# Kernel optimization log

Measured on AMD Instinct MI355X. Metric: run time of the kernel, lower is better.

Reference implementation:

```python
import jax, jax.numpy as jnp
import numpy as np

B, T, D, NH = 4, 2048, 1024, 16
HD = D // NH


def setup_inputs() -> dict:
    key = jax.random.key(0)
    ks = jax.random.split(key, 6)
    scale = 0.02
    x = jax.random.normal(ks[0], (B, T, D), dtype=jnp.float32)
    Wr = jax.random.normal(ks[1], (D, D), dtype=jnp.float32) * scale
    Wk = jax.random.normal(ks[2], (D, D), dtype=jnp.float32) * scale
    Wv = jax.random.normal(ks[3], (D, D), dtype=jnp.float32) * scale
    Ww = jax.random.normal(ks[4], (D, D), dtype=jnp.float32) * scale
    Wo = jax.random.normal(ks[5], (D, D), dtype=jnp.float32) * scale
    return {"x": x, "Wr": Wr, "Wk": Wk, "Wv": Wv, "Ww": Ww, "Wo": Wo}


def _rwkv7_forward(x, Wr, Wk, Wv, Ww, Wo):
    b, t, d = x.shape
    nh, hd = NH, d // NH
    # projections (F.linear: x @ W.T), no bias
    r = jax.nn.sigmoid(x @ Wr.T).reshape(b, t, nh, hd)
    k = (x @ Wk.T).reshape(b, t, nh, hd)
    v = (x @ Wv.T).reshape(b, t, nh, hd)
    w = (jax.nn.sigmoid(x @ Ww.T) * 0.99).reshape(b, t, nh, hd)

    def step(state, inp):
        # state: [B, nh, hd_v, hd_k]
        w_t, k_t, v_t, r_t = inp  # each [B, nh, hd]
        state = state * w_t[..., :, None] + v_t[..., :, None] * k_t[..., None, :]
        out_t = r_t * state.sum(-1)  # [B, nh, hd]
        return state, out_t

    seq = (jnp.moveaxis(w, 1, 0), jnp.moveaxis(k, 1, 0),
           jnp.moveaxis(v, 1, 0), jnp.moveaxis(r, 1, 0))  # time-major
    state0 = jnp.zeros((b, nh, hd, hd), dtype=x.dtype)
    _, outs = jax.lax.scan(step, state0, seq)  # [T, B, nh, hd]
    out = jnp.moveaxis(outs, 0, 1).reshape(b, t, d)

    # RMSNorm with eps=None -> torch uses dtype eps
    eps = jnp.asarray(jnp.finfo(out.dtype).eps, out.dtype)
    out = out * jax.lax.rsqrt(jnp.mean(out * out, axis=-1, keepdims=True) + eps)
    return out @ Wo.T


def reference(x, Wr, Wk, Wv, Ww, Wo):
    return _rwkv7_forward(x, Wr, Wk, Wv, Ww, Wo)
```

## Files before the change

### kernel.cpp

```cpp
#include <hip/hip_runtime.h>
#include <hip/hip_bf16.h>
#include <stdint.h>


#define BB 4
#define TT 2048
#define DD 1024
#define NHH 16
#define HDD 64
#define CC 64
#define LL 32
#define NCH 4096
#define MT (BB * TT)
#define ROWP 136

using bf16 = __hip_bfloat16;
typedef __attribute__((ext_vector_type(8))) short bfrag8;
typedef __attribute__((ext_vector_type(8))) unsigned short us8;
typedef __attribute__((ext_vector_type(4))) float f32x4;

__device__ __forceinline__ void async_ld16(const bf16* g, bf16* l) {
  __builtin_amdgcn_global_load_lds(
      (const __attribute__((address_space(1))) uint32_t*)g,
      (__attribute__((address_space(3))) uint32_t*)l, 16, 0, 0);
}

__device__ __forceinline__ float sigm(float x) {
  return __builtin_amdgcn_rcpf(1.0f + __expf(-x));
}
__device__ __forceinline__ float bf2f(bf16 h) {
  unsigned short u = *reinterpret_cast<unsigned short*>(&h);
  return __uint_as_float((unsigned)u << 16);
}
__device__ __forceinline__ float us2f(unsigned short u) {
  return __uint_as_float((unsigned)u << 16);
}
__device__ __forceinline__ unsigned short f2bfbits(float f) {
  bf16 b = __float2bfloat16(f);
  return *reinterpret_cast<unsigned short*>(&b);
}

__global__ __launch_bounds__(256)
void convert_kernel(const float* __restrict__ x,
                    const float* __restrict__ Wr, const float* __restrict__ Wv,
                    const float* __restrict__ Ww, const float* __restrict__ Wo,
                    const float* __restrict__ Wk,
                    bf16* __restrict__ x_c, bf16* __restrict__ W_c,
                    bf16* __restrict__ wks_bf)
{
  if (blockIdx.x < 64) {
    const int gid = blockIdx.x * 256 + threadIdx.x;
    const int h = gid >> 10, c = gid & 1023;
    float s = 0.0f;
    for (int j = 0; j < 64; ++j)
      s += Wk[(long)((h << 6) + j) * 1024 + c];
    wks_bf[gid] = __float2bfloat16(s);
    return;
  }
  const long g = (long)(blockIdx.x - 64) * 256 + threadIdx.x;
  const float* src; bf16* dst; long off4;
  if (g < 2097152) { src = x; dst = x_c; off4 = g; }
  else {
    long gg = g - 2097152;
    int wsel = (int)(gg >> 18);
    off4 = gg & 262143;
    src = (wsel == 0) ? Wr : (wsel == 1) ? Wv : (wsel == 2) ? Ww : Wo;
    dst = W_c + (long)wsel * 1048576;
  }
  float4 f = reinterpret_cast<const float4*>(src)[off4];
  ushort4 pk;
  pk.x = f2bfbits(f.x); pk.y = f2bfbits(f.y);
  pk.z = f2bfbits(f.z); pk.w = f2bfbits(f.w);
  reinterpret_cast<ushort4*>(dst)[off4] = pk;
}

__device__ __forceinline__ void gemm_mainloop(
    const bf16* __restrict__ A, const bf16* __restrict__ W,
    int blockM, int blockN, bf16* a_sh, bf16* b_sh, f32x4 acc[4][4])
{
  const int tid    = threadIdx.x;
  const int wave   = tid >> 6;
  const int lane   = tid & 63;
  const int lane15 = lane & 15;
  const int quad   = lane >> 4;
  const int waveM  = wave >> 1;
  const int waveN  = wave & 1;
  const int s_row  = (wave << 5) + (lane >> 3);
  const int s_col  = (((lane & 7) ^ ((lane >> 3) & 7)) << 3);

  const bf16* gA = A + ((long)(blockM * 128) + s_row) * 1024 + s_col;
  const bf16* gW = W + ((long)(blockN * 128) + s_row) * 1024 + s_col;
  bf16* la = a_sh + wave * 2048;
  bf16* lb = b_sh + wave * 2048;

  const int rsw = lane15 & 7;

  for (int k0 = 0; k0 < 1024; k0 += 64) {
#pragma unroll
    for (int it = 0; it < 4; ++it) {
      async_ld16(gA + k0 + it * 8 * 1024, la + it * 512);
      async_ld16(gW + k0 + it * 8 * 1024, lb + it * 512);
    }
    __syncthreads();
#pragma unroll
    for (int kh = 0; kh < 2; ++kh) {
      bfrag8 af[4], bfv[4];
      const int pc = ((kh * 4 + quad) ^ rsw) << 3;
#pragma unroll
      for (int mi = 0; mi < 4; ++mi)
        af[mi] = *reinterpret_cast<const bfrag8*>(a_sh + (waveM*64 + mi*16 + lane15)*64 + pc);
#pragma unroll
      for (int ni = 0; ni < 4; ++ni)
        bfv[ni] = *reinterpret_cast<const bfrag8*>(b_sh + (waveN*64 + ni*16 + lane15)*64 + pc);
#pragma unroll
      for (int mi = 0; mi < 4; ++mi)
#pragma unroll
        for (int ni = 0; ni < 4; ++ni)
          acc[mi][ni] = __builtin_amdgcn_mfma_f32_16x16x32_bf16(af[mi], bfv[ni], acc[mi][ni], 0, 0, 0);
    }
    __syncthreads();
  }
}

__global__ __launch_bounds__(256, 2)
void proj_kernel(const bf16* __restrict__ X, const bf16* __restrict__ W_c,
                 bf16* __restrict__ r_t, bf16* __restrict__ v_t,
                 bf16* __restrict__ w_t,
                 const bf16* __restrict__ wks_bf, float* __restrict__ ksum)
{
  __shared__ __align__(16) bf16 sh[128 * ROWP];
  const int tid = threadIdx.x;

  if (blockIdx.x < 128) {
    const int kb   = blockIdx.x;
    const int wave = tid >> 6, lane = tid & 63;
    const int m0   = (kb * 4 + wave) * 16;
    const int kc   = (lane >> 4) * 8;
    const bf16* xp = X + (long)(m0 + (lane & 15)) * DD + kc;
    const bf16* wp = wks_bf + (lane & 15) * DD + kc;
    f32x4 acc0 = {}, acc1 = {};
#pragma unroll 4
    for (int k0 = 0; k0 < 1024; k0 += 64) {
      bfrag8 a0 = *reinterpret_cast<const bfrag8*>(xp + k0);
      bfrag8 b0 = *reinterpret_cast<const bfrag8*>(wp + k0);
      bfrag8 a1 = *reinterpret_cast<const bfrag8*>(xp + k0 + 32);
      bfrag8 b1 = *reinterpret_cast<const bfrag8*>(wp + k0 + 32);
      acc0 = __builtin_amdgcn_mfma_f32_16x16x32_bf16(a0, b0, acc0, 0, 0, 0);
      acc1 = __builtin_amdgcn_mfma_f32_16x16x32_bf16(a1, b1, acc1, 0, 0, 0);
    }
    const int h = lane & 15;
#pragma unroll
    for (int r = 0; r < 4; ++r) {
      const int m = m0 + (lane >> 4) * 4 + r;
      const int b = m >> 11, t = m & (TT - 1);
      ksum[((long)(b * NHH + h)) * TT + t] = acc0[r] + acc1[r];
    }
    return;
  }

  const int f  = blockIdx.x - 128;
  const int u  = f & 7;
  const int q  = f >> 3;
  const int n  = q & 7;
  const int p  = q >> 3;
  const int mh = p & 7;
  const int mode = p >> 3;
  const int m  = u + (mh << 3);

  const bf16* W = W_c + (long)mode * 1048576;
  f32x4 acc[4][4] = {};
  gemm_mainloop(X, W, m, n, sh, sh + 8192, acc);

  const int wave = tid >> 6, lane = tid & 63;
  const int lane15 = lane & 15, quad = lane >> 4;
  const int waveM = wave >> 1, waveN = wave & 1;
  bf16* outp = (mode == 0) ? r_t : (mode == 1) ? v_t : w_t;

#pragma unroll
  for (int mi = 0; mi < 4; ++mi) {
    const int mm0 = waveM*64 + mi*16 + quad*4;
#pragma unroll
    for (int ni = 0; ni < 4; ++ni) {
      const int nn = waveN*64 + ni*16 + lane15;
      float v0 = acc[mi][ni][0], v1 = acc[mi][ni][1];
      float v2 = acc[mi][ni][2], v3 = acc[mi][ni][3];
      if (mode == 0) { v0 = sigm(v0); v1 = sigm(v1); v2 = sigm(v2); v3 = sigm(v3); }
      else if (mode == 2) {
        v0 = sigm(v0)*0.99f; v1 = sigm(v1)*0.99f;
        v2 = sigm(v2)*0.99f; v3 = sigm(v3)*0.99f;
      }
      ushort4 pk;
      pk.x = f2bfbits(v0); pk.y = f2bfbits(v1);
      pk.z = f2bfbits(v2); pk.w = f2bfbits(v3);
      *reinterpret_cast<ushort4*>(sh + nn*ROWP + mm0) = pk;
    }
  }
  __syncthreads();

  const int nn_base = n * 128;
  const int mm_base = m * 128;
#pragma unroll
  for (int pp = 0; pp < 8; ++pp) {
    const int nn_l = pp*16 + (tid >> 4);
    const int mm_l = (tid & 15) * 8;
    us8 v = *reinterpret_cast<const us8*>(sh + nn_l*ROWP + mm_l);
    *reinterpret_cast<us8*>(outp + (long)(nn_base + nn_l) * MT + (mm_base + mm_l)) = v;
  }
}

__global__ __launch_bounds__(256)
void scanA_kernel(const bf16* __restrict__ v_t, const bf16* __restrict__ w_t,
                  const float* __restrict__ ksum,
                  float* __restrict__ Pbuf, float* __restrict__ Abuf)
{
  __shared__ float ks_sh[128];
  const int bh = blockIdx.x;
  const int b = bh >> 4, h = bh & 15;
  const int tid = threadIdx.x;
  const int i = tid & 63;
  const int cg = tid >> 6;
  const int chunk = blockIdx.y * 4 + cg;
  if (tid < 128) ks_sh[tid] = ksum[(long)bh * TT + blockIdx.y * 128 + tid];
  __syncthreads();
  const int ch = h * HDD + i;
  const long tbase = (long)ch * MT + b * TT + chunk * LL;
  us8 wv[4], vv[4];
#pragma unroll
  for (int q = 0; q < 4; ++q) {
    wv[q] = *reinterpret_cast<const us8*>(w_t + tbase + q*8);
    vv[q] = *reinterpret_cast<const us8*>(v_t + tbase + q*8);
  }
  const float* ksp = ks_sh + cg * LL;
  float s = 0.0f, P = 1.0f;
#pragma unroll
  for (int j = 0; j < LL; ++j) {
    float wf = us2f((unsigned short)wv[j>>3][j&7]);
    float vf = us2f((unsigned short)vv[j>>3][j&7]);
    s = fmaf(wf, s, vf * ksp[j]);
    P *= wf;
  }
  const int chn = bh * 64 + i;
  Pbuf[chunk * NCH + chn] = P;
  Abuf[chunk * NCH + chn] = s;
}

__global__ __launch_bounds__(256)
void scanB_kernel(const float* __restrict__ Pbuf, float* __restrict__ Abuf,
                  float* __restrict__ rowssq)
{
  const int tid  = threadIdx.x;
  const int lane = tid & 63;
  const int wch  = blockIdx.x * 4 + (tid >> 6);
  const int idx  = lane * NCH + wch;
  float p = Pbuf[idx];
  float a = Abuf[idx];
#pragma unroll
  for (int d = 1; d < 64; d <<= 1) {
    float al = __shfl_up(a, d);
    float pl = __shfl_up(p, d);
    if (lane >= d) { a = fmaf(p, al, a); p *= pl; }
  }
  float carry = __shfl_up(a, 1);
  if (lane == 0) carry = 0.0f;
  Abuf[idx] = carry;
  if (blockIdx.x < 32) rowssq[blockIdx.x * 256 + tid] = 0.0f;
}

__global__ __launch_bounds__(256)
void scanC_kernel(const bf16* __restrict__ r_t, const bf16* __restrict__ v_t,
                  const bf16* __restrict__ w_t, const float* __restrict__ ksum,
                  const float* __restrict__ Abuf, bf16* __restrict__ so,
                  float* __restrict__ rowssq)
{
  __shared__ float ks_sh[128];
  const int bh = blockIdx.x;
  const int b = bh >> 4, h = bh & 15;
  const int tid = threadIdx.x;
  const int i = tid & 63;
  const int cg = tid >> 6;
  const int chunk = blockIdx.y * 4 + cg;
  if (tid < 128) ks_sh[tid] = ksum[(long)bh * TT + blockIdx.y * 128 + tid];
  __syncthreads();
  const int ch = h * HDD + i;
  const long tbase = (long)ch * MT + b * TT + chunk * LL;
  us8 wv[4], vv[4], rv[4];
#pragma unroll
  for (int q = 0; q < 4; ++q) {
    wv[q] = *reinterpret_cast<const us8*>(w_t + tbase + q*8);
    vv[q] = *reinterpret_cast<const us8*>(v_t + tbase + q*8);
    rv[q] = *reinterpret_cast<const us8*>(r_t + tbase + q*8);
  }
  const float* ksp = ks_sh + cg * LL;
  const int chn = bh * 64 + i;
  float s = Abuf[chunk * NCH + chn];
  const long obase = (long)(b * TT + chunk * LL) * DD + ch;
#pragma unroll
  for (int j = 0; j < LL; ++j) {
    float wf = us2f((unsigned short)wv[j>>3][j&7]);
    float vf = us2f((unsigned short)vv[j>>3][j&7]);
    float rf = us2f((unsigned short)rv[j>>3][j&7]);
    s = fmaf(wf, s, vf * ksp[j]);
    unsigned short ob = f2bfbits(rf * s);
    *reinterpret_cast<unsigned short*>(so + obase + (long)j * DD) = ob;
    float vfo = us2f(ob);
    float ss = vfo * vfo;
#pragma unroll
    for (int msk = 1; msk <= 32; msk <<= 1) ss += __shfl_xor(ss, msk);
    if (i == 0) atomicAdd(&rowssq[b * TT + chunk * LL + j], ss);
  }
}

__global__ __launch_bounds__(256, 2)
void out_gemm_kernel(const bf16* __restrict__ A, const bf16* __restrict__ Wo_c,
                     const float* __restrict__ rowssq, float* __restrict__ out)
{
  __shared__ __align__(16) bf16 a_sh[128*64];
  __shared__ __align__(16) bf16 b_sh[128*64];
  const int f  = blockIdx.x;
  const int u  = f & 7;
  const int q  = f >> 3;
  const int n  = q & 7;
  const int mh = q >> 3;
  const int m  = u + (mh << 3);

  f32x4 acc[4][4] = {};
  gemm_mainloop(A, Wo_c, m, n, a_sh, b_sh, acc);

  const int tid = threadIdx.x;
  const int wave = tid >> 6, lane = tid & 63;
  const int lane15 = lane & 15, quad = lane >> 4;
  const int waveM = wave >> 1, waveN = wave & 1;
  const int m_base = m * 128 + waveM * 64;
  const int n_base = n * 128 + waveN * 64;
#pragma unroll
  for (int mi = 0; mi < 4; ++mi)
#pragma unroll
    for (int r = 0; r < 4; ++r) {
      int mm = m_base + mi*16 + quad*4 + r;
      float sc = rsqrtf(rowssq[mm] * (1.0f / DD) + 1.1920929e-07f);
#pragma unroll
      for (int ni = 0; ni < 4; ++ni) {
        int nn = n_base + ni*16 + lane15;
        out[(long)mm * DD + nn] = acc[mi][ni][r] * sc;
      }
    }
}

extern "C" void kernel_launch(void* const* d_in, const int* in_sizes, int n_in,
                              void* d_out, int out_size, void* d_ws, size_t ws_size,
                              hipStream_t stream) {
  const float* x  = (const float*)d_in[0];
  const float* Wr = (const float*)d_in[1];
  const float* Wk = (const float*)d_in[2];
  const float* Wv = (const float*)d_in[3];
  const float* Ww = (const float*)d_in[4];
  const float* Wo = (const float*)d_in[5];

  const long NELT = (long)BB * TT * DD;
  bf16*  x_c  = (bf16*)d_ws;
  bf16*  W_c  = x_c + NELT;
  bf16*  v_t  = W_c + 4 * 1048576;
  float* ksum = (float*)(v_t + NELT);
  bf16*  wks_bf = (bf16*)(ksum + (long)BB * NHH * TT);
  float* Pbuf = (float*)(wks_bf + NHH * DD) + 8192;
  float* Abuf = Pbuf + (long)CC * NCH;
  float* rowssq = (float*)W_c;

  bf16*  r_t  = (bf16*)d_out;
  bf16*  w_t  = (bf16*)d_out + NELT;
  bf16*  so   = x_c;
  float* out  = (float*)d_out;

  convert_kernel<<<dim3(12352), 256, 0, stream>>>(x, Wr, Wv, Ww, Wo, Wk, x_c, W_c, wks_bf);
  proj_kernel<<<dim3(1664), 256, 0, stream>>>(x_c, W_c, r_t, v_t, w_t, wks_bf, ksum);
  scanA_kernel<<<dim3(64, 16), 256, 0, stream>>>(v_t, w_t, ksum, Pbuf, Abuf);
  scanB_kernel<<<dim3(1024), 256, 0, stream>>>(Pbuf, Abuf, rowssq);
  scanC_kernel<<<dim3(64, 16), 256, 0, stream>>>(r_t, v_t, w_t, ksum, Abuf, so, rowssq);
  out_gemm_kernel<<<dim3(512), 256, 0, stream>>>(so, W_c + 3 * 1048576, rowssq, out);
}
```

Before: 216.4 us.

## Compute RMSNorm row sums inside output GEMM and coarsen convert kernel

Removes the per-timestep wave reduction and global atomicAdd of squared outputs from the scan kernel. Each output GEMM block now computes the row sum of squares itself from the A fragments it already loads into registers, reduces them across lanes and keeps them in shared memory. Also drops the rowssq zeroing in scanB, and makes the convert kernel handle four float4 elements per thread with a quarter of the blocks. The cost is redundant ALU work in the GEMM mainloop, since every N-block recomputes the same row norms, plus an extra shared array and barrier.

```diff
diff --git a/kernel.cpp b/kernel.cpp
--- a/kernel.cpp
+++ b/kernel.cpp
@@ -57,21 +57,25 @@
     wks_bf[gid] = __float2bfloat16(s);
     return;
   }
-  const long g = (long)(blockIdx.x - 64) * 256 + threadIdx.x;
-  const float* src; bf16* dst; long off4;
-  if (g < 2097152) { src = x; dst = x_c; off4 = g; }
-  else {
-    long gg = g - 2097152;
-    int wsel = (int)(gg >> 18);
-    off4 = gg & 262143;
-    src = (wsel == 0) ? Wr : (wsel == 1) ? Wv : (wsel == 2) ? Ww : Wo;
-    dst = W_c + (long)wsel * 1048576;
-  }
-  float4 f = reinterpret_cast<const float4*>(src)[off4];
-  ushort4 pk;
-  pk.x = f2bfbits(f.x); pk.y = f2bfbits(f.y);
-  pk.z = f2bfbits(f.z); pk.w = f2bfbits(f.w);
-  reinterpret_cast<ushort4*>(dst)[off4] = pk;
+  const long g0 = (long)(blockIdx.x - 64) * 1024 + threadIdx.x;
+#pragma unroll
+  for (int it = 0; it < 4; ++it) {
+    const long g = g0 + it * 256;
+    const float* src; bf16* dst; long off4;
+    if (g < 2097152) { src = x; dst = x_c; off4 = g; }
+    else {
+      long gg = g - 2097152;
+      int wsel = (int)(gg >> 18);
+      off4 = gg & 262143;
+      src = (wsel == 0) ? Wr : (wsel == 1) ? Wv : (wsel == 2) ? Ww : Wo;
+      dst = W_c + (long)wsel * 1048576;
+    }
+    float4 f = reinterpret_cast<const float4*>(src)[off4];
+    ushort4 pk;
+    pk.x = f2bfbits(f.x); pk.y = f2bfbits(f.y);
+    pk.z = f2bfbits(f.z); pk.w = f2bfbits(f.w);
+    reinterpret_cast<ushort4*>(dst)[off4] = pk;
+  }
 }
 
 __device__ __forceinline__ void gemm_mainloop(
@@ -120,6 +124,71 @@
     }
     __syncthreads();
   }
+}
+
+__device__ __forceinline__ void gemm_mainloop_ssq(
+    const bf16* __restrict__ A, const bf16* __restrict__ W,
+    int blockM, int blockN, bf16* a_sh, bf16* b_sh, f32x4 acc[4][4],
+    float* sh_ssq)
+{
+  const int tid    = threadIdx.x;
+  const int wave   = tid >> 6;
+  const int lane   = tid & 63;
+  const int lane15 = lane & 15;
+  const int quad   = lane >> 4;
+  const int waveM  = wave >> 1;
+  const int waveN  = wave & 1;
+  const int s_row  = (wave << 5) + (lane >> 3);
+  const int s_col  = (((lane & 7) ^ ((lane >> 3) & 7)) << 3);
+
+  const bf16* gA = A + ((long)(blockM * 128) + s_row) * 1024 + s_col;
+  const bf16* gW = W + ((long)(blockN * 128) + s_row) * 1024 + s_col;
+  bf16* la = a_sh + wave * 2048;
+  bf16* lb = b_sh + wave * 2048;
+
+  const int rsw = lane15 & 7;
+  float ssq0 = 0.0f, ssq1 = 0.0f;
+
+  for (int k0 = 0; k0 < 1024; k0 += 64) {
+#pragma unroll
+    for (int it = 0; it < 4; ++it) {
+      async_ld16(gA + k0 + it * 8 * 1024, la + it * 512);
+      async_ld16(gW + k0 + it * 8 * 1024, lb + it * 512);
+    }
+    __syncthreads();
+#pragma unroll
+    for (int kh = 0; kh < 2; ++kh) {
+      bfrag8 af[4], bfv[4];
+      const int pc = ((kh * 4 + quad) ^ rsw) << 3;
+#pragma unroll
+      for (int mi = 0; mi < 4; ++mi)
+        af[mi] = *reinterpret_cast<const bfrag8*>(a_sh + (waveM*64 + mi*16 + lane15)*64 + pc);
+#pragma unroll
+      for (int ni = 0; ni < 4; ++ni)
+        bfv[ni] = *reinterpret_cast<const bfrag8*>(b_sh + (waveN*64 + ni*16 + lane15)*64 + pc);
+#pragma unroll
+      for (int e = 0; e < 8; ++e) {
+        float f0 = us2f((unsigned short)af[waveN*2 + 0][e]);
+        float f1 = us2f((unsigned short)af[waveN*2 + 1][e]);
+        ssq0 = fmaf(f0, f0, ssq0);
+        ssq1 = fmaf(f1, f1, ssq1);
+      }
+#pragma unroll
+      for (int mi = 0; mi < 4; ++mi)
+#pragma unroll
+        for (int ni = 0; ni < 4; ++ni)
+          acc[mi][ni] = __builtin_amdgcn_mfma_f32_16x16x32_bf16(af[mi], bfv[ni], acc[mi][ni], 0, 0, 0);
+    }
+    __syncthreads();
+  }
+
+  ssq0 += __shfl_xor(ssq0, 16); ssq0 += __shfl_xor(ssq0, 32);
+  ssq1 += __shfl_xor(ssq1, 16); ssq1 += __shfl_xor(ssq1, 32);
+  if (quad == 0) {
+    sh_ssq[waveM*64 + (waveN*2 + 0)*16 + lane15] = ssq0;
+    sh_ssq[waveM*64 + (waveN*2 + 1)*16 + lane15] = ssq1;
+  }
+  __syncthreads();
 }
 
 __global__ __launch_bounds__(256, 2)
@@ -245,8 +314,7 @@
 }
 
 __global__ __launch_bounds__(256)
-void scanB_kernel(const float* __restrict__ Pbuf, float* __restrict__ Abuf,
-                  float* __restrict__ rowssq)
+void scanB_kernel(const float* __restrict__ Pbuf, float* __restrict__ Abuf)
 {
   const int tid  = threadIdx.x;
   const int lane = tid & 63;
@@ -263,14 +331,12 @@
   float carry = __shfl_up(a, 1);
   if (lane == 0) carry = 0.0f;
   Abuf[idx] = carry;
-  if (blockIdx.x < 32) rowssq[blockIdx.x * 256 + tid] = 0.0f;
 }
 
 __global__ __launch_bounds__(256)
 void scanC_kernel(const bf16* __restrict__ r_t, const bf16* __restrict__ v_t,
                   const bf16* __restrict__ w_t, const float* __restrict__ ksum,
-                  const float* __restrict__ Abuf, bf16* __restrict__ so,
-                  float* __restrict__ rowssq)
+                  const float* __restrict__ Abuf, bf16* __restrict__ so)
 {
   __shared__ float ks_sh[128];
   const int bh = blockIdx.x;
@@ -300,22 +366,17 @@
     float vf = us2f((unsigned short)vv[j>>3][j&7]);
     float rf = us2f((unsigned short)rv[j>>3][j&7]);
     s = fmaf(wf, s, vf * ksp[j]);
-    unsigned short ob = f2bfbits(rf * s);
-    *reinterpret_cast<unsigned short*>(so + obase + (long)j * DD) = ob;
-    float vfo = us2f(ob);
-    float ss = vfo * vfo;
-#pragma unroll
-    for (int msk = 1; msk <= 32; msk <<= 1) ss += __shfl_xor(ss, msk);
-    if (i == 0) atomicAdd(&rowssq[b * TT + chunk * LL + j], ss);
+    *reinterpret_cast<unsigned short*>(so + obase + (long)j * DD) = f2bfbits(rf * s);
   }
 }
 
 __global__ __launch_bounds__(256, 2)
 void out_gemm_kernel(const bf16* __restrict__ A, const bf16* __restrict__ Wo_c,
-                     const float* __restrict__ rowssq, float* __restrict__ out)
+                     float* __restrict__ out)
 {
   __shared__ __align__(16) bf16 a_sh[128*64];
   __shared__ __align__(16) bf16 b_sh[128*64];
+  __shared__ float sh_ssq[128];
   const int f  = blockIdx.x;
   const int u  = f & 7;
   const int q  = f >> 3;
@@ -324,7 +385,7 @@
   const int m  = u + (mh << 3);
 
   f32x4 acc[4][4] = {};
-  gemm_mainloop(A, Wo_c, m, n, a_sh, b_sh, acc);
+  gemm_mainloop_ssq(A, Wo_c, m, n, a_sh, b_sh, acc, sh_ssq);
 
   const int tid = threadIdx.x;
   const int wave = tid >> 6, lane = tid & 63;
@@ -336,8 +397,9 @@
   for (int mi = 0; mi < 4; ++mi)
 #pragma unroll
     for (int r = 0; r < 4; ++r) {
-      int mm = m_base + mi*16 + quad*4 + r;
-      float sc = rsqrtf(rowssq[mm] * (1.0f / DD) + 1.1920929e-07f);
+      int loc = waveM*64 + mi*16 + quad*4 + r;
+      int mm = m * 128 + loc;
+      float sc = rsqrtf(sh_ssq[loc] * (1.0f / DD) + 1.1920929e-07f);
 #pragma unroll
       for (int ni = 0; ni < 4; ++ni) {
         int nn = n_base + ni*16 + lane15;
@@ -364,17 +426,16 @@
   bf16*  wks_bf = (bf16*)(ksum + (long)BB * NHH * TT);
   float* Pbuf = (float*)(wks_bf + NHH * DD) + 8192;
   float* Abuf = Pbuf + (long)CC * NCH;
-  float* rowssq = (float*)W_c;
 
   bf16*  r_t  = (bf16*)d_out;
   bf16*  w_t  = (bf16*)d_out + NELT;
   bf16*  so   = x_c;
   float* out  = (float*)d_out;
 
-  convert_kernel<<<dim3(12352), 256, 0, stream>>>(x, Wr, Wv, Ww, Wo, Wk, x_c, W_c, wks_bf);
+  convert_kernel<<<dim3(3136), 256, 0, stream>>>(x, Wr, Wv, Ww, Wo, Wk, x_c, W_c, wks_bf);
   proj_kernel<<<dim3(1664), 256, 0, stream>>>(x_c, W_c, r_t, v_t, w_t, wks_bf, ksum);
   scanA_kernel<<<dim3(64, 16), 256, 0, stream>>>(v_t, w_t, ksum, Pbuf, Abuf);
-  scanB_kernel<<<dim3(1024), 256, 0, stream>>>(Pbuf, Abuf, rowssq);
-  scanC_kernel<<<dim3(64, 16), 256, 0, stream>>>(r_t, v_t, w_t, ksum, Abuf, so, rowssq);
-  out_gemm_kernel<<<dim3(512), 256, 0, stream>>>(so, W_c + 3 * 1048576, rowssq, out);
-}
+  scanB_kernel<<<dim3(1024), 256, 0, stream>>>(Pbuf, Abuf);
+  scanC_kernel<<<dim3(64, 16), 256, 0, stream>>>(r_t, v_t, w_t, ksum, Abuf, so);
+  out_gemm_kernel<<<dim3(512), 256, 0, stream>>>(so, W_c + 3 * 1048576, out);
+}
```

Result: slower. 289.9 us (+34.0%).
